# Performance work log

Hardware: AMD Instinct MI355X
Metric: run time of the kernel (lower is better)

## Reference

```python
import jax, jax.numpy as jnp
import numpy as np
from jax.ops import segment_sum, segment_max

N, E, IN_DIM, HID, HEADS, B, ACTIONS = 16384, 262144, 512, 256, 4, 64, 32
NEG_SLOPE = 0.2  # PyG GATConv default leaky-relu slope


def setup_inputs() -> dict:
    key = jax.random.key(0)
    ks = jax.random.split(key, 12)
    x = jax.random.normal(ks[0], (N, IN_DIM), dtype=jnp.float32)
    edge_index = jax.random.randint(ks[1], (2, E), 0, N, dtype=jnp.int64)
    batch = jnp.sort(jax.random.randint(ks[2], (N,), 0, B, dtype=jnp.int64))
    s = 0.05
    return {
        "x": x,
        "edge_index": edge_index,
        "batch": batch,
        # SAGEConv: lin_l (neighbors, with bias) + lin_r (root, no bias)
        "sage_w_l": jax.random.normal(ks[3], (IN_DIM, HID), dtype=jnp.float32) * s,
        "sage_b_l": jnp.zeros((HID,), dtype=jnp.float32),
        "sage_w_r": jax.random.normal(ks[4], (IN_DIM, HID), dtype=jnp.float32) * s,
        # GATConv: shared lin, per-head attention vectors, output bias (concat=False)
        "gat_w": jax.random.normal(ks[5], (HID, HEADS * HID), dtype=jnp.float32) * s,
        "gat_att_src": jax.random.normal(ks[6], (HEADS, HID), dtype=jnp.float32) * s,
        "gat_att_dst": jax.random.normal(ks[7], (HEADS, HID), dtype=jnp.float32) * s,
        "gat_b": jnp.zeros((HID,), dtype=jnp.float32),
        # action head
        "head_w": jax.random.normal(ks[8], (HID, ACTIONS), dtype=jnp.float32) * s,
        "head_b": jnp.zeros((ACTIONS,), dtype=jnp.float32),
    }


def reference(x, edge_index, batch, sage_w_l, sage_b_l, sage_w_r,
              gat_w, gat_att_src, gat_att_dst, gat_b, head_w, head_b):
    src, dst = edge_index[0], edge_index[1]

    # ---- SAGEConv (mean aggregation): lin_l(mean_j x_j) + lin_r(x_i) ----
    agg = segment_sum(x[src], dst, num_segments=N)                 # [N, IN_DIM]
    deg = segment_sum(jnp.ones((E,), x.dtype), dst, num_segments=N)
    mean_nbr = agg / jnp.maximum(deg, 1.0)[:, None]
    h = mean_nbr @ sage_w_l + sage_b_l + x @ sage_w_r              # [N, HID]
    h = jax.nn.relu(h)
    # dropout is identity at inference (training=False)

    # ---- GATConv (adds self-loops, concat=False -> head average) ----
    loop = jnp.arange(N, dtype=src.dtype)
    si = jnp.concatenate([src, loop])                              # [E2]
    di = jnp.concatenate([dst, loop])
    g = (h @ gat_w).reshape(N, HEADS, HID)                         # [N, H, C]
    a_src = jnp.einsum('nhc,hc->nh', g, gat_att_src)               # [N, H]
    a_dst = jnp.einsum('nhc,hc->nh', g, gat_att_dst)
    logits = jax.nn.leaky_relu(a_src[si] + a_dst[di], NEG_SLOPE)   # [E2, H]
    m = segment_max(logits, di, num_segments=N)                    # per-target max
    ex = jnp.exp(logits - m[di])
    denom = segment_sum(ex, di, num_segments=N)
    alpha = ex / denom[di]                                         # [E2, H]
    out = segment_sum(g[si] * alpha[:, :, None], di, num_segments=N)  # [N, H, C]
    out = jax.nn.relu(out.mean(axis=1) + gat_b)                    # [N, HID]

    # ---- global mean pool + action head ----
    pooled = segment_sum(out, batch, num_segments=B)
    cnt = segment_sum(jnp.ones((N,), out.dtype), batch, num_segments=B)
    pooled = pooled / jnp.maximum(cnt, 1.0)[:, None]               # [B, HID]
    return pooled @ head_w + head_b                                # [B, ACTIONS]
```

## Files before the change

kernel.cpp:

```cpp
#include <hip/hip_runtime.h>
#include <math.h>

#define N_NODES 16384
#define N_EDGES 262144
#define IN_DIM  512
#define HID     256
#define HEADS   4
#define NBATCH  64
#define ACTIONS 32
#define NEG_SLOPE 0.2f

typedef __attribute__((ext_vector_type(8))) short short8;
typedef __attribute__((ext_vector_type(4))) float f32x4;

__device__ __forceinline__ float lrelu(float v) { return v > 0.f ? v : NEG_SLOPE * v; }

__device__ __forceinline__ unsigned short bf16_rne(float f) {
    union { float f; unsigned int u; } x; x.f = f;
    unsigned int u = x.u;
    unsigned int r = (u + 0x7FFFu + ((u >> 16) & 1u)) >> 16;
    return (unsigned short)r;
}

__device__ __forceinline__ float bf16_to_f32(unsigned short s) {
    union { unsigned int u; float f; } x; x.u = (unsigned int)s << 16;
    return x.f;
}

__device__ __forceinline__ float4 bf4_to_f4(ushort4 u) {
    return make_float4(bf16_to_f32(u.x), bf16_to_f32(u.y), bf16_to_f32(u.z), bf16_to_f32(u.w));
}

__device__ __forceinline__ void async_copy16(const unsigned short* g, unsigned short* l) {
    __builtin_amdgcn_global_load_lds(
        (const __attribute__((address_space(1))) unsigned int*)g,
        (__attribute__((address_space(3))) unsigned int*)l, 16, 0, 0);
}

__global__ void zero_int_kernel(int* __restrict__ p, int n) {
    int i = blockIdx.x * 256 + threadIdx.x;
    if (i < n) p[i] = 0;
}

__global__ void zero_f32_kernel(float* __restrict__ p, int n) {
    int i = blockIdx.x * 256 + threadIdx.x;
    if (i < n) p[i] = 0.f;
}

__global__ void f32_to_bf16_kernel(const float* __restrict__ in, unsigned short* __restrict__ out, int n) {
    int i = (blockIdx.x * 256 + threadIdx.x) * 4;
    if (i < n) {
        float4 v = *(const float4*)(in + i);
        ushort4 o;
        o.x = bf16_rne(v.x); o.y = bf16_rne(v.y); o.z = bf16_rne(v.z); o.w = bf16_rne(v.w);
        *(ushort4*)(out + i) = o;
    }
}

__global__ void pack_wlr_bt_kernel(const float* __restrict__ wl, const float* __restrict__ wr,
                                   unsigned short* __restrict__ bt) {
    int idx = blockIdx.x * 256 + threadIdx.x;
    int j = idx >> 9;
    int k = idx & 511;
    float v = (j < HID) ? wl[k * HID + j] : wr[k * HID + (j - HID)];
    bt[idx] = bf16_rne(v);
}

__global__ void pack_wstack_bt_kernel(const float* __restrict__ gat_w, unsigned short* __restrict__ bt) {
    int idx = blockIdx.x * 256 + threadIdx.x;
    int c = idx >> 10;
    int r = idx & 1023;
    int h = r >> 8;
    int k = r & 255;
    bt[idx] = bf16_rne(gat_w[(size_t)k * (HEADS * HID) + h * HID + c]);
}

__global__ void watt_kernel(const float* __restrict__ gat_w,
                            const float* __restrict__ att_src,
                            const float* __restrict__ att_dst,
                            float* __restrict__ watt) {
    int j = blockIdx.x;
    int c = threadIdx.x;
    int hh = j & 3;
    const float* att = (j < 4) ? (att_src + hh * HID) : (att_dst + hh * HID);
    float s = 0.f;
    for (int cc = 0; cc < HID; cc++)
        s += gat_w[(size_t)c * (HEADS * HID) + hh * HID + cc] * att[cc];
    watt[j * HID + c] = s;
}

__global__ void deg_kernel(const int* __restrict__ ei, int* __restrict__ deg) {
    int e = blockIdx.x * 256 + threadIdx.x;
    if (e < N_EDGES) atomicAdd(&deg[ei[N_EDGES + e]], 1);
}

__global__ void scan_kernel(const int* __restrict__ deg, int* __restrict__ row_start,
                            int* __restrict__ pos) {
    __shared__ int part[256];
    int t = threadIdx.x;
    int base = t * 64;
    int s = 0;
    for (int i = 0; i < 64; i++) s += deg[base + i];
    part[t] = s;
    __syncthreads();
    if (t == 0) {
        int acc = 0;
        for (int i = 0; i < 256; i++) { int v = part[i]; part[i] = acc; acc += v; }
    }
    __syncthreads();
    int run = part[t];
    for (int i = 0; i < 64; i++) {
        row_start[base + i] = run;
        pos[base + i] = run;
        run += deg[base + i];
    }
    if (t == 255) row_start[N_NODES] = run;
}

__global__ void fill_kernel(const int* __restrict__ ei, int* __restrict__ pos,
                            int* __restrict__ col) {
    int e = blockIdx.x * 256 + threadIdx.x;
    if (e < N_EDGES) {
        int s = ei[e];
        int d = ei[N_EDGES + e];
        int p = atomicAdd(&pos[d], 1);
        col[p] = s;
    }
}

#define BM 128
#define BN 128
#define BK 32

__global__ __launch_bounds__(256) void gemm_bt_kernel(const unsigned short* __restrict__ A,
                                                      const unsigned short* __restrict__ Bt,
                                                      float* __restrict__ Cf,
                                                      unsigned short* __restrict__ Cb,
                                                      int M, int Nn, int K,
                                                      const float* __restrict__ bias,
                                                      float scale, int mode) {
    __shared__ __align__(16) unsigned short As[BM * BK];
    __shared__ __align__(16) unsigned short Bs[BN * BK];

    int tid  = threadIdx.x;
    int wv   = tid >> 6;
    int lane = tid & 63;
    int m0 = blockIdx.y * BM;
    int n0 = blockIdx.x * BN;
    int wm = (wv & 1) * 64;
    int wn = (wv >> 1) * 64;

    int srow = tid >> 2;
    int scol = (tid & 3) * 8;
    const unsigned short* Ag0 = A  + (size_t)(m0 + srow) * K + scol;
    const unsigned short* Ag1 = A  + (size_t)(m0 + 64 + srow) * K + scol;
    const unsigned short* Bg0 = Bt + (size_t)(n0 + srow) * K + scol;
    const unsigned short* Bg1 = Bt + (size_t)(n0 + 64 + srow) * K + scol;
    unsigned short* Al0 = As + wv * 512;
    unsigned short* Al1 = As + 2048 + wv * 512;
    unsigned short* Bl0 = Bs + wv * 512;
    unsigned short* Bl1 = Bs + 2048 + wv * 512;

    int fr   = lane & 15;
    int fk   = (lane >> 4) * 8;
    f32x4 acc[4][4] = {};

    for (int kt = 0; kt < K; kt += BK) {
        async_copy16(Ag0 + kt, Al0);
        async_copy16(Ag1 + kt, Al1);
        async_copy16(Bg0 + kt, Bl0);
        async_copy16(Bg1 + kt, Bl1);
        __syncthreads();

        short8 af[4], bf[4];
#pragma unroll
        for (int mi = 0; mi < 4; mi++)
            af[mi] = *(const short8*)&As[(wm + mi * 16 + fr) * BK + fk];
#pragma unroll
        for (int ni = 0; ni < 4; ni++)
            bf[ni] = *(const short8*)&Bs[(wn + ni * 16 + fr) * BK + fk];
#pragma unroll
        for (int mi = 0; mi < 4; mi++)
#pragma unroll
            for (int ni = 0; ni < 4; ni++)
                acc[mi][ni] = __builtin_amdgcn_mfma_f32_16x16x32_bf16(af[mi], bf[ni], acc[mi][ni], 0, 0, 0);
        __syncthreads();
    }

    int cr = (lane >> 4) * 4;
    int cc = lane & 15;
#pragma unroll
    for (int mi = 0; mi < 4; mi++) {
#pragma unroll
        for (int ni = 0; ni < 4; ni++) {
            int gc = n0 + wn + ni * 16 + cc;
            float b = (mode == 1) ? bias[gc] : 0.f;
#pragma unroll
            for (int r = 0; r < 4; r++) {
                int gr = m0 + wm + mi * 16 + cr + r;
                float v = acc[mi][ni][r];
                if (mode == 1) {
                    Cf[(size_t)gr * Nn + gc] = fmaxf(fmaf(v, scale, b), 0.f);
                } else {
                    Cb[(size_t)gr * Nn + gc] = bf16_rne(v);
                }
            }
        }
    }
}

__global__ __launch_bounds__(256) void sage_agg_kernel(const unsigned short* __restrict__ xlr,
                                                       const int* __restrict__ row_start,
                                                       const int* __restrict__ col,
                                                       const float* __restrict__ b_l,
                                                       const float* __restrict__ watt,
                                                       unsigned short* __restrict__ hb,
                                                       float* __restrict__ a_att) {
    __shared__ float watt_s[8 * HID];
    for (int i = threadIdx.x; i < 8 * HID; i += 256) watt_s[i] = watt[i];
    __syncthreads();

    int wave = threadIdx.x >> 6;
    int lane = threadIdx.x & 63;
    int n = blockIdx.x * 4 + wave;
    int start = row_start[n], end = row_start[n + 1];
    int c0 = lane * 4;

    float4 acc = make_float4(0.f, 0.f, 0.f, 0.f);
    int e = start;
    for (; e + 4 <= end; e += 4) {
        int s0 = col[e], s1 = col[e + 1], s2 = col[e + 2], s3 = col[e + 3];
        ushort4 u0 = *(const ushort4*)(xlr + (size_t)s0 * IN_DIM + c0);
        ushort4 u1 = *(const ushort4*)(xlr + (size_t)s1 * IN_DIM + c0);
        ushort4 u2 = *(const ushort4*)(xlr + (size_t)s2 * IN_DIM + c0);
        ushort4 u3 = *(const ushort4*)(xlr + (size_t)s3 * IN_DIM + c0);
        float4 v0 = bf4_to_f4(u0), v1 = bf4_to_f4(u1), v2 = bf4_to_f4(u2), v3 = bf4_to_f4(u3);
        acc.x += (v0.x + v1.x) + (v2.x + v3.x);
        acc.y += (v0.y + v1.y) + (v2.y + v3.y);
        acc.z += (v0.z + v1.z) + (v2.z + v3.z);
        acc.w += (v0.w + v1.w) + (v2.w + v3.w);
    }
    for (; e < end; e++) {
        int s = col[e];
        float4 v = bf4_to_f4(*(const ushort4*)(xlr + (size_t)s * IN_DIM + c0));
        acc.x += v.x; acc.y += v.y; acc.z += v.z; acc.w += v.w;
    }
    float inv = 1.f / (float)max(end - start, 1);
    float4 xr = bf4_to_f4(*(const ushort4*)(xlr + (size_t)n * IN_DIM + HID + c0));
    float4 bl = *(const float4*)(b_l + c0);
    float4 hv;
    hv.x = fmaxf(fmaf(acc.x, inv, bl.x + xr.x), 0.f);
    hv.y = fmaxf(fmaf(acc.y, inv, bl.y + xr.y), 0.f);
    hv.z = fmaxf(fmaf(acc.z, inv, bl.z + xr.z), 0.f);
    hv.w = fmaxf(fmaf(acc.w, inv, bl.w + xr.w), 0.f);
    ushort4 ho;
    ho.x = bf16_rne(hv.x); ho.y = bf16_rne(hv.y); ho.z = bf16_rne(hv.z); ho.w = bf16_rne(hv.w);
    *(ushort4*)(hb + (size_t)n * HID + c0) = ho;

    float p[8];
#pragma unroll
    for (int j = 0; j < 8; j++) {
        float4 wt = *(const float4*)&watt_s[j * HID + c0];
        p[j] = hv.x * wt.x + hv.y * wt.y + hv.z * wt.z + hv.w * wt.w;
    }
#pragma unroll
    for (int off = 32; off; off >>= 1)
#pragma unroll
        for (int j = 0; j < 8; j++) p[j] += __shfl_down(p[j], off);
    if (lane == 0) {
#pragma unroll
        for (int j = 0; j < 8; j++) a_att[n * 8 + j] = p[j];
    }
}

__global__ __launch_bounds__(256) void gat_agg_kernel(const unsigned short* __restrict__ hb,
                                                      const float* __restrict__ a_att,
                                                      const int* __restrict__ row_start,
                                                      const int* __restrict__ col,
                                                      unsigned short* __restrict__ T) {
    __shared__ __align__(16) float w_s[4][64 * 4];
    int wave = threadIdx.x >> 6;
    int lane = threadIdx.x & 63;
    int n = blockIdx.x * 4 + wave;
    int start = row_start[n], end = row_start[n + 1];

    float4 an = *(const float4*)(a_att + n * 8);
    float4 ad = *(const float4*)(a_att + n * 8 + 4);
    float adst[4] = {ad.x, ad.y, ad.z, ad.w};
    float selfl[4], m[4];
    {
        float asn[4] = {an.x, an.y, an.z, an.w};
#pragma unroll
        for (int hh = 0; hh < 4; hh++) {
            selfl[hh] = lrelu(asn[hh] + adst[hh]);
            m[hh] = -INFINITY;
        }
    }
    for (int e = start + lane; e < end; e += 64) {
        int s = col[e];
        float4 as = *(const float4*)(a_att + s * 8);
        m[0] = fmaxf(m[0], lrelu(as.x + adst[0]));
        m[1] = fmaxf(m[1], lrelu(as.y + adst[1]));
        m[2] = fmaxf(m[2], lrelu(as.z + adst[2]));
        m[3] = fmaxf(m[3], lrelu(as.w + adst[3]));
    }
#pragma unroll
    for (int off = 32; off; off >>= 1)
#pragma unroll
        for (int hh = 0; hh < 4; hh++) m[hh] = fmaxf(m[hh], __shfl_down(m[hh], off));
#pragma unroll
    for (int hh = 0; hh < 4; hh++) {
        m[hh] = __shfl(m[hh], 0);
        m[hh] = fmaxf(m[hh], selfl[hh]);
    }
    float d[4] = {0.f, 0.f, 0.f, 0.f};
    for (int e = start + lane; e < end; e += 64) {
        int s = col[e];
        float4 as = *(const float4*)(a_att + s * 8);
        d[0] += __expf(lrelu(as.x + adst[0]) - m[0]);
        d[1] += __expf(lrelu(as.y + adst[1]) - m[1]);
        d[2] += __expf(lrelu(as.z + adst[2]) - m[2]);
        d[3] += __expf(lrelu(as.w + adst[3]) - m[3]);
    }
#pragma unroll
    for (int off = 32; off; off >>= 1)
#pragma unroll
        for (int hh = 0; hh < 4; hh++) d[hh] += __shfl_down(d[hh], off);
    float invd[4];
#pragma unroll
    for (int hh = 0; hh < 4; hh++) {
        d[hh] = __shfl(d[hh], 0) + __expf(selfl[hh] - m[hh]);
        invd[hh] = 1.f / d[hh];
    }

    int c0 = lane * 4;
    float4 hn = bf4_to_f4(*(const ushort4*)(hb + (size_t)n * HID + c0));
    float4 acc[4];
#pragma unroll
    for (int hh = 0; hh < 4; hh++) {
        float ws = __expf(selfl[hh] - m[hh]) * invd[hh];
        acc[hh] = make_float4(ws * hn.x, ws * hn.y, ws * hn.z, ws * hn.w);
    }
    for (int base = start; base < end; base += 64) {
        int cnt = min(64, end - base);
        if (lane < cnt) {
            int s = col[base + lane];
            float4 as = *(const float4*)(a_att + s * 8);
            float4 wv;
            wv.x = __expf(lrelu(as.x + adst[0]) - m[0]) * invd[0];
            wv.y = __expf(lrelu(as.y + adst[1]) - m[1]) * invd[1];
            wv.z = __expf(lrelu(as.z + adst[2]) - m[2]) * invd[2];
            wv.w = __expf(lrelu(as.w + adst[3]) - m[3]) * invd[3];
            *(float4*)&w_s[wave][lane * 4] = wv;
        }
        __builtin_amdgcn_wave_barrier();

        int i = 0;
        for (; i + 2 <= cnt; i += 2) {
            int s0 = col[base + i], s1 = col[base + i + 1];
            float4 w0 = *(const float4*)&w_s[wave][i * 4];
            float4 w1 = *(const float4*)&w_s[wave][(i + 1) * 4];
            ushort4 u0 = *(const ushort4*)(hb + (size_t)s0 * HID + c0);
            ushort4 u1 = *(const ushort4*)(hb + (size_t)s1 * HID + c0);
            float4 h0 = bf4_to_f4(u0), h1 = bf4_to_f4(u1);
            float wr0[4] = {w0.x, w0.y, w0.z, w0.w};
            float wr1[4] = {w1.x, w1.y, w1.z, w1.w};
#pragma unroll
            for (int hh = 0; hh < 4; hh++) {
                acc[hh].x = fmaf(wr0[hh], h0.x, fmaf(wr1[hh], h1.x, acc[hh].x));
                acc[hh].y = fmaf(wr0[hh], h0.y, fmaf(wr1[hh], h1.y, acc[hh].y));
                acc[hh].z = fmaf(wr0[hh], h0.z, fmaf(wr1[hh], h1.z, acc[hh].z));
                acc[hh].w = fmaf(wr0[hh], h0.w, fmaf(wr1[hh], h1.w, acc[hh].w));
            }
        }
        if (i < cnt) {
            int s0 = col[base + i];
            float4 w0 = *(const float4*)&w_s[wave][i * 4];
            float4 h0 = bf4_to_f4(*(const ushort4*)(hb + (size_t)s0 * HID + c0));
            float wr0[4] = {w0.x, w0.y, w0.z, w0.w};
#pragma unroll
            for (int hh = 0; hh < 4; hh++) {
                acc[hh].x = fmaf(wr0[hh], h0.x, acc[hh].x);
                acc[hh].y = fmaf(wr0[hh], h0.y, acc[hh].y);
                acc[hh].z = fmaf(wr0[hh], h0.z, acc[hh].z);
                acc[hh].w = fmaf(wr0[hh], h0.w, acc[hh].w);
            }
        }
        __builtin_amdgcn_wave_barrier();
    }
#pragma unroll
    for (int hh = 0; hh < 4; hh++) {
        ushort4 o;
        o.x = bf16_rne(acc[hh].x); o.y = bf16_rne(acc[hh].y);
        o.z = bf16_rne(acc[hh].z); o.w = bf16_rne(acc[hh].w);
        *(ushort4*)(T + (size_t)n * (HEADS * HID) + hh * HID + c0) = o;
    }
}

__global__ __launch_bounds__(256) void pool_partial_kernel(const float* __restrict__ outn,
                                                           const int* __restrict__ batch,
                                                           float* __restrict__ pooled) {
    int c = threadIdx.x;
    int n0 = blockIdx.x * 64;
    int cur = batch[n0];
    float acc = 0.f;
    for (int i = 0; i < 64; i++) {
        int n = n0 + i;
        int b = batch[n];
        if (b != cur) {
            atomicAdd(&pooled[cur * HID + c], acc);
            acc = 0.f;
            cur = b;
        }
        acc += outn[(size_t)n * HID + c];
    }
    atomicAdd(&pooled[cur * HID + c], acc);
}

__device__ __forceinline__ int lower_bound_i(const int* a, int n, int v) {
    int lo = 0, hi = n;
    while (lo < hi) {
        int mid = (lo + hi) >> 1;
        if (a[mid] < v) lo = mid + 1; else hi = mid;
    }
    return lo;
}

__global__ __launch_bounds__(256) void head_kernel(const float* __restrict__ pooled,
                                                   const int* __restrict__ batch,
                                                   const float* __restrict__ head_w,
                                                   const float* __restrict__ head_b,
                                                   float* __restrict__ out) {
    __shared__ float sm[HID];
    int b = blockIdx.x;
    int c = threadIdx.x;
    int lo = lower_bound_i(batch, N_NODES, b);
    int hi = lower_bound_i(batch, N_NODES, b + 1);
    int cnt = hi - lo;
    sm[c] = pooled[b * HID + c] / (float)max(cnt, 1);
    __syncthreads();
    if (c < ACTIONS) {
        float acc = head_b[c];
        for (int k = 0; k < HID; k++) acc = fmaf(sm[k], head_w[k * ACTIONS + c], acc);
        out[b * ACTIONS + c] = acc;
    }
}

extern "C" void kernel_launch(void* const* d_in, const int* in_sizes, int n_in,
                              void* d_out, int out_size, void* d_ws, size_t ws_size,
                              hipStream_t stream) {
    const float* x        = (const float*)d_in[0];
    const int*   ei       = (const int*)d_in[1];
    const int*   batch    = (const int*)d_in[2];
    const float* sage_w_l = (const float*)d_in[3];
    const float* sage_b_l = (const float*)d_in[4];
    const float* sage_w_r = (const float*)d_in[5];
    const float* gat_w    = (const float*)d_in[6];
    const float* att_src  = (const float*)d_in[7];
    const float* att_dst  = (const float*)d_in[8];
    const float* gat_b    = (const float*)d_in[9];
    const float* head_w   = (const float*)d_in[10];
    const float* head_b   = (const float*)d_in[11];
    float* out = (float*)d_out;

    char* w = (char*)d_ws;
    float* outn   = (float*)w; w += (size_t)N_NODES * HID * 4;
    float* a_att  = (float*)w; w += (size_t)N_NODES * 8 * 4;
    float* watt   = (float*)w; w += (size_t)8 * HID * 4;
    float* pooled = (float*)w; w += (size_t)NBATCH * HID * 4;
    unsigned short* xb  = (unsigned short*)w; w += (size_t)N_NODES * IN_DIM * 2;
    unsigned short* xlr = (unsigned short*)w; w += (size_t)N_NODES * IN_DIM * 2;
    unsigned short* hb  = (unsigned short*)w; w += (size_t)N_NODES * HID * 2;
    unsigned short* T   = (unsigned short*)w; w += (size_t)N_NODES * HEADS * HID * 2;
    unsigned short* bt1 = (unsigned short*)w; w += (size_t)(2 * HID) * IN_DIM * 2;
    unsigned short* bt2 = (unsigned short*)w; w += (size_t)HID * (HEADS * HID) * 2;
    int* deg      = (int*)w;   w += (size_t)N_NODES * 4;
    int* row_start= (int*)w;   w += (size_t)(N_NODES + 64) * 4;
    int* pos      = (int*)w;   w += (size_t)N_NODES * 4;
    int* col      = (int*)w;   w += (size_t)N_EDGES * 4;

    f32_to_bf16_kernel<<<(N_NODES * IN_DIM / 4) / 256, 256, 0, stream>>>(x, xb, N_NODES * IN_DIM);
    pack_wlr_bt_kernel<<<(2 * HID * IN_DIM) / 256, 256, 0, stream>>>(sage_w_l, sage_w_r, bt1);
    pack_wstack_bt_kernel<<<(HID * HEADS * HID) / 256, 256, 0, stream>>>(gat_w, bt2);
    watt_kernel<<<8, 256, 0, stream>>>(gat_w, att_src, att_dst, watt);

    zero_int_kernel<<<(N_NODES + 255) / 256, 256, 0, stream>>>(deg, N_NODES);
    deg_kernel<<<N_EDGES / 256, 256, 0, stream>>>(ei, deg);
    scan_kernel<<<1, 256, 0, stream>>>(deg, row_start, pos);
    fill_kernel<<<N_EDGES / 256, 256, 0, stream>>>(ei, pos, col);
    zero_f32_kernel<<<(NBATCH * HID) / 256, 256, 0, stream>>>(pooled, NBATCH * HID);

    gemm_bt_kernel<<<dim3((2 * HID) / BN, N_NODES / BM), 256, 0, stream>>>(
        xb, bt1, nullptr, xlr, N_NODES, 2 * HID, IN_DIM, nullptr, 1.f, 0);

    sage_agg_kernel<<<N_NODES / 4, 256, 0, stream>>>(xlr, row_start, col, sage_b_l, watt, hb, a_att);

    gat_agg_kernel<<<N_NODES / 4, 256, 0, stream>>>(hb, a_att, row_start, col, T);

    gemm_bt_kernel<<<dim3(HID / BN, N_NODES / BM), 256, 0, stream>>>(
        T, bt2, outn, nullptr, N_NODES, HID, HEADS * HID, gat_b, 0.25f, 1);

    pool_partial_kernel<<<N_NODES / 64, 256, 0, stream>>>(outn, batch, pooled);
    head_kernel<<<NBATCH, 256, 0, stream>>>(pooled, batch, head_w, head_b, out);
}
```

Measured before the change: 302.2 us.

## Fuse setup kernels, single-pass GAT softmax, fuse GEMM with mean pooling

Merges the conversion, weight-packing, attention-weight and zeroing kernels into one launch to cut launch overhead. Replaces the serial scan with a wave-shuffle scan that uses vectorized int4 loads. Drops the two extra edge passes of the GAT softmax: each edge weight is exponentiated against a fixed shift (the larger of the self logit and zero) and normalized at the end, which gives up the guarantee against exp overflow when neighbor logits are large. Fuses the second GEMM epilogue with global mean pooling through atomics, removing the fp32 node-output buffer and the separate pool kernel.

```diff
diff --git a/kernel.cpp b/kernel.cpp
--- a/kernel.cpp
+++ b/kernel.cpp
@@ -37,56 +37,53 @@
         (__attribute__((address_space(3))) unsigned int*)l, 16, 0, 0);
 }
 
-__global__ void zero_int_kernel(int* __restrict__ p, int n) {
-    int i = blockIdx.x * 256 + threadIdx.x;
-    if (i < n) p[i] = 0;
-}
-
-__global__ void zero_f32_kernel(float* __restrict__ p, int n) {
-    int i = blockIdx.x * 256 + threadIdx.x;
-    if (i < n) p[i] = 0.f;
-}
-
-__global__ void f32_to_bf16_kernel(const float* __restrict__ in, unsigned short* __restrict__ out, int n) {
-    int i = (blockIdx.x * 256 + threadIdx.x) * 4;
-    if (i < n) {
-        float4 v = *(const float4*)(in + i);
+#define NB_CONV 8192
+#define NB_WLR  1024
+#define NB_WSTK 1024
+#define NB_WATT 8
+#define NB_ZERO 128
+#define NB_SETUP (NB_CONV + NB_WLR + NB_WSTK + NB_WATT + NB_ZERO)
+
+__global__ __launch_bounds__(256) void setup_kernel(
+        const float* __restrict__ x, unsigned short* __restrict__ xb,
+        const float* __restrict__ wl, const float* __restrict__ wr, unsigned short* __restrict__ bt1,
+        const float* __restrict__ gat_w, unsigned short* __restrict__ bt2,
+        const float* __restrict__ att_src, const float* __restrict__ att_dst, float* __restrict__ watt,
+        int* __restrict__ deg, float* __restrict__ pooled) {
+    int bid = blockIdx.x, tid = threadIdx.x;
+    if (bid < NB_CONV) {
+        int i = (bid * 256 + tid) * 4;
+        float4 v = *(const float4*)(x + i);
         ushort4 o;
         o.x = bf16_rne(v.x); o.y = bf16_rne(v.y); o.z = bf16_rne(v.z); o.w = bf16_rne(v.w);
-        *(ushort4*)(out + i) = o;
-    }
-}
-
-__global__ void pack_wlr_bt_kernel(const float* __restrict__ wl, const float* __restrict__ wr,
-                                   unsigned short* __restrict__ bt) {
-    int idx = blockIdx.x * 256 + threadIdx.x;
-    int j = idx >> 9;
-    int k = idx & 511;
-    float v = (j < HID) ? wl[k * HID + j] : wr[k * HID + (j - HID)];
-    bt[idx] = bf16_rne(v);
-}
-
-__global__ void pack_wstack_bt_kernel(const float* __restrict__ gat_w, unsigned short* __restrict__ bt) {
-    int idx = blockIdx.x * 256 + threadIdx.x;
-    int c = idx >> 10;
-    int r = idx & 1023;
-    int h = r >> 8;
-    int k = r & 255;
-    bt[idx] = bf16_rne(gat_w[(size_t)k * (HEADS * HID) + h * HID + c]);
-}
-
-__global__ void watt_kernel(const float* __restrict__ gat_w,
-                            const float* __restrict__ att_src,
-                            const float* __restrict__ att_dst,
-                            float* __restrict__ watt) {
-    int j = blockIdx.x;
-    int c = threadIdx.x;
-    int hh = j & 3;
-    const float* att = (j < 4) ? (att_src + hh * HID) : (att_dst + hh * HID);
-    float s = 0.f;
-    for (int cc = 0; cc < HID; cc++)
-        s += gat_w[(size_t)c * (HEADS * HID) + hh * HID + cc] * att[cc];
-    watt[j * HID + c] = s;
+        *(ushort4*)(xb + i) = o;
+    } else if (bid < NB_CONV + NB_WLR) {
+        int idx = (bid - NB_CONV) * 256 + tid;
+        int j = idx >> 9;
+        int k = idx & 511;
+        float v = (j < HID) ? wl[k * HID + j] : wr[k * HID + (j - HID)];
+        bt1[idx] = bf16_rne(v);
+    } else if (bid < NB_CONV + NB_WLR + NB_WSTK) {
+        int idx = (bid - NB_CONV - NB_WLR) * 256 + tid;
+        int c = idx >> 10;
+        int r = idx & 1023;
+        int h = r >> 8;
+        int k = r & 255;
+        bt2[idx] = bf16_rne(gat_w[(size_t)k * (HEADS * HID) + h * HID + c]);
+    } else if (bid < NB_CONV + NB_WLR + NB_WSTK + NB_WATT) {
+        int j = bid - NB_CONV - NB_WLR - NB_WSTK;
+        int c = tid;
+        int hh = j & 3;
+        const float* att = (j < 4) ? (att_src + hh * HID) : (att_dst + hh * HID);
+        float s = 0.f;
+        for (int cc = 0; cc < HID; cc++)
+            s += gat_w[(size_t)c * (HEADS * HID) + hh * HID + cc] * att[cc];
+        watt[j * HID + c] = s;
+    } else {
+        int idx = (bid - NB_CONV - NB_WLR - NB_WSTK - NB_WATT) * 256 + tid;
+        if (idx < N_NODES) deg[idx] = 0;
+        else pooled[idx - N_NODES] = 0.f;
+    }
 }
 
 __global__ void deg_kernel(const int* __restrict__ ei, int* __restrict__ deg) {
@@ -94,25 +91,41 @@
     if (e < N_EDGES) atomicAdd(&deg[ei[N_EDGES + e]], 1);
 }
 
-__global__ void scan_kernel(const int* __restrict__ deg, int* __restrict__ row_start,
-                            int* __restrict__ pos) {
-    __shared__ int part[256];
+__global__ __launch_bounds__(256) void scan_kernel(const int* __restrict__ deg,
+                                                   int* __restrict__ row_start,
+                                                   int* __restrict__ pos) {
     int t = threadIdx.x;
+    int lane = t & 63, wv = t >> 6;
     int base = t * 64;
-    int s = 0;
-    for (int i = 0; i < 64; i++) s += deg[base + i];
-    part[t] = s;
+    int4 buf[16];
+    int sum = 0;
+#pragma unroll
+    for (int i = 0; i < 16; i++) {
+        buf[i] = ((const int4*)(deg + base))[i];
+        sum += buf[i].x + buf[i].y + buf[i].z + buf[i].w;
+    }
+    int v = sum;
+#pragma unroll
+    for (int off = 1; off < 64; off <<= 1) {
+        int u = __shfl_up(v, off);
+        if (lane >= off) v += u;
+    }
+    __shared__ int wsum[4];
+    if (lane == 63) wsum[wv] = v;
     __syncthreads();
-    if (t == 0) {
-        int acc = 0;
-        for (int i = 0; i < 256; i++) { int v = part[i]; part[i] = acc; acc += v; }
-    }
-    __syncthreads();
-    int run = part[t];
-    for (int i = 0; i < 64; i++) {
-        row_start[base + i] = run;
-        pos[base + i] = run;
-        run += deg[base + i];
+    int wbase = 0;
+    for (int w0 = 0; w0 < wv; w0++) wbase += wsum[w0];
+    int run = wbase + v - sum;
+#pragma unroll
+    for (int i = 0; i < 16; i++) {
+        int4 b = buf[i];
+        int4 o;
+        o.x = run; run += b.x;
+        o.y = run; run += b.y;
+        o.z = run; run += b.z;
+        o.w = run; run += b.w;
+        ((int4*)(row_start + base))[i] = o;
+        ((int4*)(pos + base))[i] = o;
     }
     if (t == 255) row_start[N_NODES] = run;
 }
@@ -134,11 +147,8 @@
 
 __global__ __launch_bounds__(256) void gemm_bt_kernel(const unsigned short* __restrict__ A,
                                                       const unsigned short* __restrict__ Bt,
-                                                      float* __restrict__ Cf,
                                                       unsigned short* __restrict__ Cb,
-                                                      int M, int Nn, int K,
-                                                      const float* __restrict__ bias,
-                                                      float scale, int mode) {
+                                                      int Nn, int K) {
     __shared__ __align__(16) unsigned short As[BM * BK];
     __shared__ __align__(16) unsigned short Bs[BN * BK];
 
@@ -161,8 +171,8 @@
     unsigned short* Bl0 = Bs + wv * 512;
     unsigned short* Bl1 = Bs + 2048 + wv * 512;
 
-    int fr   = lane & 15;
-    int fk   = (lane >> 4) * 8;
+    int fr = lane & 15;
+    int fk = (lane >> 4) * 8;
     f32x4 acc[4][4] = {};
 
     for (int kt = 0; kt < K; kt += BK) {
@@ -194,16 +204,94 @@
 #pragma unroll
         for (int ni = 0; ni < 4; ni++) {
             int gc = n0 + wn + ni * 16 + cc;
-            float b = (mode == 1) ? bias[gc] : 0.f;
 #pragma unroll
             for (int r = 0; r < 4; r++) {
                 int gr = m0 + wm + mi * 16 + cr + r;
-                float v = acc[mi][ni][r];
-                if (mode == 1) {
-                    Cf[(size_t)gr * Nn + gc] = fmaxf(fmaf(v, scale, b), 0.f);
-                } else {
-                    Cb[(size_t)gr * Nn + gc] = bf16_rne(v);
-                }
+                Cb[(size_t)gr * Nn + gc] = bf16_rne(acc[mi][ni][r]);
+            }
+        }
+    }
+}
+
+__global__ __launch_bounds__(256) void gemm_bt_pool_kernel(const unsigned short* __restrict__ A,
+                                                           const unsigned short* __restrict__ Bt,
+                                                           const int* __restrict__ batch,
+                                                           const float* __restrict__ bias,
+                                                           float scale,
+                                                           float* __restrict__ pooled,
+                                                           int Nn, int K) {
+    __shared__ __align__(16) unsigned short As[BM * BK];
+    __shared__ __align__(16) unsigned short Bs[BN * BK];
+    __shared__ int bsh[BM];
+
+    int tid  = threadIdx.x;
+    int wv   = tid >> 6;
+    int lane = tid & 63;
+    int m0 = blockIdx.y * BM;
+    int n0 = blockIdx.x * BN;
+    int wm = (wv & 1) * 64;
+    int wn = (wv >> 1) * 64;
+
+    if (tid < BM) bsh[tid] = batch[m0 + tid];
+
+    int srow = tid >> 2;
+    int scol = (tid & 3) * 8;
+    const unsigned short* Ag0 = A  + (size_t)(m0 + srow) * K + scol;
+    const unsigned short* Ag1 = A  + (size_t)(m0 + 64 + srow) * K + scol;
+    const unsigned short* Bg0 = Bt + (size_t)(n0 + srow) * K + scol;
+    const unsigned short* Bg1 = Bt + (size_t)(n0 + 64 + srow) * K + scol;
+    unsigned short* Al0 = As + wv * 512;
+    unsigned short* Al1 = As + 2048 + wv * 512;
+    unsigned short* Bl0 = Bs + wv * 512;
+    unsigned short* Bl1 = Bs + 2048 + wv * 512;
+
+    int fr = lane & 15;
+    int fk = (lane >> 4) * 8;
+    f32x4 acc[4][4] = {};
+
+    for (int kt = 0; kt < K; kt += BK) {
+        async_copy16(Ag0 + kt, Al0);
+        async_copy16(Ag1 + kt, Al1);
+        async_copy16(Bg0 + kt, Bl0);
+        async_copy16(Bg1 + kt, Bl1);
+        __syncthreads();
+
+        short8 af[4], bf[4];
+#pragma unroll
+        for (int mi = 0; mi < 4; mi++)
+            af[mi] = *(const short8*)&As[(wm + mi * 16 + fr) * BK + fk];
+#pragma unroll
+        for (int ni = 0; ni < 4; ni++)
+            bf[ni] = *(const short8*)&Bs[(wn + ni * 16 + fr) * BK + fk];
+#pragma unroll
+        for (int mi = 0; mi < 4; mi++)
+#pragma unroll
+            for (int ni = 0; ni < 4; ni++)
+                acc[mi][ni] = __builtin_amdgcn_mfma_f32_16x16x32_bf16(af[mi], bf[ni], acc[mi][ni], 0, 0, 0);
+        __syncthreads();
+    }
+
+    int cr = (lane >> 4) * 4;
+    int cc = lane & 15;
+#pragma unroll
+    for (int mi = 0; mi < 4; mi++) {
+        int rowb = wm + mi * 16 + cr;
+        int b0 = bsh[rowb], b3 = bsh[rowb + 3];
+#pragma unroll
+        for (int ni = 0; ni < 4; ni++) {
+            int gc = n0 + wn + ni * 16 + cc;
+            float b = bias[gc];
+            float v0 = fmaxf(fmaf(acc[mi][ni][0], scale, b), 0.f);
+            float v1 = fmaxf(fmaf(acc[mi][ni][1], scale, b), 0.f);
+            float v2 = fmaxf(fmaf(acc[mi][ni][2], scale, b), 0.f);
+            float v3 = fmaxf(fmaf(acc[mi][ni][3], scale, b), 0.f);
+            if (b0 == b3) {
+                atomicAdd(&pooled[b0 * HID + gc], (v0 + v1) + (v2 + v3));
+            } else {
+                atomicAdd(&pooled[bsh[rowb + 0] * HID + gc], v0);
+                atomicAdd(&pooled[bsh[rowb + 1] * HID + gc], v1);
+                atomicAdd(&pooled[bsh[rowb + 2] * HID + gc], v2);
+                atomicAdd(&pooled[bsh[rowb + 3] * HID + gc], v3);
             }
         }
     }
@@ -287,71 +375,35 @@
     float4 an = *(const float4*)(a_att + n * 8);
     float4 ad = *(const float4*)(a_att + n * 8 + 4);
     float adst[4] = {ad.x, ad.y, ad.z, ad.w};
-    float selfl[4], m[4];
-    {
-        float asn[4] = {an.x, an.y, an.z, an.w};
-#pragma unroll
-        for (int hh = 0; hh < 4; hh++) {
-            selfl[hh] = lrelu(asn[hh] + adst[hh]);
-            m[hh] = -INFINITY;
-        }
-    }
-    for (int e = start + lane; e < end; e += 64) {
-        int s = col[e];
-        float4 as = *(const float4*)(a_att + s * 8);
-        m[0] = fmaxf(m[0], lrelu(as.x + adst[0]));
-        m[1] = fmaxf(m[1], lrelu(as.y + adst[1]));
-        m[2] = fmaxf(m[2], lrelu(as.z + adst[2]));
-        m[3] = fmaxf(m[3], lrelu(as.w + adst[3]));
-    }
-#pragma unroll
-    for (int off = 32; off; off >>= 1)
-#pragma unroll
-        for (int hh = 0; hh < 4; hh++) m[hh] = fmaxf(m[hh], __shfl_down(m[hh], off));
+    float selfl[4] = {lrelu(an.x + ad.x), lrelu(an.y + ad.y), lrelu(an.z + ad.z), lrelu(an.w + ad.w)};
+    float m[4], wself[4];
 #pragma unroll
     for (int hh = 0; hh < 4; hh++) {
-        m[hh] = __shfl(m[hh], 0);
-        m[hh] = fmaxf(m[hh], selfl[hh]);
-    }
-    float d[4] = {0.f, 0.f, 0.f, 0.f};
-    for (int e = start + lane; e < end; e += 64) {
-        int s = col[e];
-        float4 as = *(const float4*)(a_att + s * 8);
-        d[0] += __expf(lrelu(as.x + adst[0]) - m[0]);
-        d[1] += __expf(lrelu(as.y + adst[1]) - m[1]);
-        d[2] += __expf(lrelu(as.z + adst[2]) - m[2]);
-        d[3] += __expf(lrelu(as.w + adst[3]) - m[3]);
-    }
-#pragma unroll
-    for (int off = 32; off; off >>= 1)
-#pragma unroll
-        for (int hh = 0; hh < 4; hh++) d[hh] += __shfl_down(d[hh], off);
-    float invd[4];
-#pragma unroll
-    for (int hh = 0; hh < 4; hh++) {
-        d[hh] = __shfl(d[hh], 0) + __expf(selfl[hh] - m[hh]);
-        invd[hh] = 1.f / d[hh];
+        m[hh] = fmaxf(selfl[hh], 0.f);
+        wself[hh] = __expf(selfl[hh] - m[hh]);
     }
 
     int c0 = lane * 4;
     float4 hn = bf4_to_f4(*(const ushort4*)(hb + (size_t)n * HID + c0));
     float4 acc[4];
 #pragma unroll
-    for (int hh = 0; hh < 4; hh++) {
-        float ws = __expf(selfl[hh] - m[hh]) * invd[hh];
-        acc[hh] = make_float4(ws * hn.x, ws * hn.y, ws * hn.z, ws * hn.w);
-    }
+    for (int hh = 0; hh < 4; hh++)
+        acc[hh] = make_float4(wself[hh] * hn.x, wself[hh] * hn.y, wself[hh] * hn.z, wself[hh] * hn.w);
+
+    float dpart[4] = {0.f, 0.f, 0.f, 0.f};
+
     for (int base = start; base < end; base += 64) {
         int cnt = min(64, end - base);
         if (lane < cnt) {
             int s = col[base + lane];
             float4 as = *(const float4*)(a_att + s * 8);
             float4 wv;
-            wv.x = __expf(lrelu(as.x + adst[0]) - m[0]) * invd[0];
-            wv.y = __expf(lrelu(as.y + adst[1]) - m[1]) * invd[1];
-            wv.z = __expf(lrelu(as.z + adst[2]) - m[2]) * invd[2];
-            wv.w = __expf(lrelu(as.w + adst[3]) - m[3]) * invd[3];
+            wv.x = __expf(lrelu(as.x + adst[0]) - m[0]);
+            wv.y = __expf(lrelu(as.y + adst[1]) - m[1]);
+            wv.z = __expf(lrelu(as.z + adst[2]) - m[2]);
+            wv.w = __expf(lrelu(as.w + adst[3]) - m[3]);
             *(float4*)&w_s[wave][lane * 4] = wv;
+            dpart[0] += wv.x; dpart[1] += wv.y; dpart[2] += wv.z; dpart[3] += wv.w;
         }
         __builtin_amdgcn_wave_barrier();
 
@@ -388,33 +440,23 @@
         }
         __builtin_amdgcn_wave_barrier();
     }
+
+#pragma unroll
+    for (int off = 32; off; off >>= 1)
+#pragma unroll
+        for (int hh = 0; hh < 4; hh++) dpart[hh] += __shfl_down(dpart[hh], off);
+    float invd[4];
+#pragma unroll
+    for (int hh = 0; hh < 4; hh++)
+        invd[hh] = 1.f / (__shfl(dpart[hh], 0) + wself[hh]);
+
 #pragma unroll
     for (int hh = 0; hh < 4; hh++) {
         ushort4 o;
-        o.x = bf16_rne(acc[hh].x); o.y = bf16_rne(acc[hh].y);
-        o.z = bf16_rne(acc[hh].z); o.w = bf16_rne(acc[hh].w);
+        o.x = bf16_rne(acc[hh].x * invd[hh]); o.y = bf16_rne(acc[hh].y * invd[hh]);
+        o.z = bf16_rne(acc[hh].z * invd[hh]); o.w = bf16_rne(acc[hh].w * invd[hh]);
         *(ushort4*)(T + (size_t)n * (HEADS * HID) + hh * HID + c0) = o;
     }
-}
-
-__global__ __launch_bounds__(256) void pool_partial_kernel(const float* __restrict__ outn,
-                                                           const int* __restrict__ batch,
-                                                           float* __restrict__ pooled) {
-    int c = threadIdx.x;
-    int n0 = blockIdx.x * 64;
-    int cur = batch[n0];
-    float acc = 0.f;
-    for (int i = 0; i < 64; i++) {
-        int n = n0 + i;
-        int b = batch[n];
-        if (b != cur) {
-            atomicAdd(&pooled[cur * HID + c], acc);
-            acc = 0.f;
-            cur = b;
-        }
-        acc += outn[(size_t)n * HID + c];
-    }
-    atomicAdd(&pooled[cur * HID + c], acc);
 }
 
 __device__ __forceinline__ int lower_bound_i(const int* a, int n, int v) {
@@ -464,7 +506,6 @@
     float* out = (float*)d_out;
 
     char* w = (char*)d_ws;
-    float* outn   = (float*)w; w += (size_t)N_NODES * HID * 4;
     float* a_att  = (float*)w; w += (size_t)N_NODES * 8 * 4;
     float* watt   = (float*)w; w += (size_t)8 * HID * 4;
     float* pooled = (float*)w; w += (size_t)NBATCH * HID * 4;
@@ -479,27 +520,23 @@
     int* pos      = (int*)w;   w += (size_t)N_NODES * 4;
     int* col      = (int*)w;   w += (size_t)N_EDGES * 4;
 
-    f32_to_bf16_kernel<<<(N_NODES * IN_DIM / 4) / 256, 256, 0, stream>>>(x, xb, N_NODES * IN_DIM);
-    pack_wlr_bt_kernel<<<(2 * HID * IN_DIM) / 256, 256, 0, stream>>>(sage_w_l, sage_w_r, bt1);
-    pack_wstack_bt_kernel<<<(HID * HEADS * HID) / 256, 256, 0, stream>>>(gat_w, bt2);
-    watt_kernel<<<8, 256, 0, stream>>>(gat_w, att_src, att_dst, watt);
-
-    zero_int_kernel<<<(N_NODES + 255) / 256, 256, 0, stream>>>(deg, N_NODES);
+    setup_kernel<<<NB_SETUP, 256, 0, stream>>>(x, xb, sage_w_l, sage_w_r, bt1,
+                                               gat_w, bt2, att_src, att_dst, watt,
+                                               deg, pooled);
+
     deg_kernel<<<N_EDGES / 256, 256, 0, stream>>>(ei, deg);
     scan_kernel<<<1, 256, 0, stream>>>(deg, row_start, pos);
     fill_kernel<<<N_EDGES / 256, 256, 0, stream>>>(ei, pos, col);
-    zero_f32_kernel<<<(NBATCH * HID) / 256, 256, 0, stream>>>(pooled, NBATCH * HID);
 
     gemm_bt_kernel<<<dim3((2 * HID) / BN, N_NODES / BM), 256, 0, stream>>>(
-        xb, bt1, nullptr, xlr, N_NODES, 2 * HID, IN_DIM, nullptr, 1.f, 0);
+        xb, bt1, xlr, 2 * HID, IN_DIM);
 
     sage_agg_kernel<<<N_NODES / 4, 256, 0, stream>>>(xlr, row_start, col, sage_b_l, watt, hb, a_att);
 
     gat_agg_kernel<<<N_NODES / 4, 256, 0, stream>>>(hb, a_att, row_start, col, T);
 
-    gemm_bt_kernel<<<dim3(HID / BN, N_NODES / BM), 256, 0, stream>>>(
-        T, bt2, outn, nullptr, N_NODES, HID, HEADS * HID, gat_b, 0.25f, 1);
-
-    pool_partial_kernel<<<N_NODES / 64, 256, 0, stream>>>(outn, batch, pooled);
+    gemm_bt_pool_kernel<<<dim3(HID / BN, N_NODES / BM), 256, 0, stream>>>(
+        T, bt2, batch, gat_b, 0.25f, pooled, HID, HEADS * HID);
+
     head_kernel<<<NBATCH, 256, 0, stream>>>(pooled, batch, head_w, head_b, out);
 }
```

Result: faster. 262.4 us (-13.2%).
